# Kernel optimization log

Measured on AMD Instinct MI355X. Metric: run time of the kernel, lower is better.

Reference implementation:

```python
import jax, jax.numpy as jnp
import numpy as np

B, T, D, H, L = 2048, 512, 8, 20, 10  # batch, seq, input_dim, hidden_dim, num_layers


def setup_inputs() -> dict:
    key = jax.random.key(0)
    ks = jax.random.split(key, 10)
    s = 1.0 / np.sqrt(H)  # PyTorch nn.RNN / nn.Linear init bound
    u = lambda k, shape: jax.random.uniform(k, shape, jnp.float32, -s, s)
    return {
        "x": jax.random.normal(ks[0], (B, T, D), jnp.float32),
        "w_ih0": u(ks[1], (H, D)),        # layer-0 input weights
        "w_ih": u(ks[2], (L - 1, H, H)),  # layers 1..9 input weights
        "w_hh": u(ks[3], (L, H, H)),
        "b_ih": u(ks[4], (L, H)),
        "b_hh": u(ks[5], (L, H)),
        "fc_w": u(ks[6], (H, H)),
        "fc_b": u(ks[7], (H,)),
        "l2_w": u(ks[8], (1, H)),
        "l2_b": u(ks[9], (1,)),
    }


def reference(x, w_ih0, w_ih, w_hh, b_ih, b_hh, fc_w, fc_b, l2_w, l2_b):
    # 10-layer Elman RNN (tanh), batch_first, h0 = 0, eval mode (no dropout).
    Bn = x.shape[0]
    h0 = jnp.zeros((L, Bn, H), x.dtype)

    def step(h, x_t):  # h: [L, B, H], x_t: [B, D]
        hs = []
        inp = x_t
        for l in range(L):  # fixed small layer count -> unrolled
            Wi = w_ih0 if l == 0 else w_ih[l - 1]
            hl = jnp.tanh(inp @ Wi.T + b_ih[l] + h[l] @ w_hh[l].T + b_hh[l])
            hs.append(hl)
            inp = hl
        return jnp.stack(hs), hl  # carry, top-layer output

    _, out = jax.lax.scan(step, h0, jnp.swapaxes(x, 0, 1))  # out: [T, B, H]
    out = jnp.swapaxes(out, 0, 1)  # [B, T, H]
    # Time-independent MLP head (original loops over t; batched here, same math)
    y = jax.nn.relu(out @ fc_w.T + fc_b) @ l2_w.T + l2_b  # [B, T, 1]
    return y
```

## Files before the change

kernel.cpp:

```cpp
#include <hip/hip_runtime.h>

#if __has_builtin(__builtin_amdgcn_exp2f)
#define EXP2F(x) __builtin_amdgcn_exp2f(x)
#else
#define EXP2F(x) exp2f(x)
#endif
#if __has_builtin(__builtin_amdgcn_rcpf)
#define RCPF(x) __builtin_amdgcn_rcpf(x)
#else
#define RCPF(x) (1.0f / (x))
#endif

namespace {

constexpr int B_ = 2048, T_ = 512, D_ = 8, H_ = 20, L_ = 10;
constexpr int NG    = 16;
constexpr int PADK  = 40;
constexpr int NW    = 11;
constexpr int NTHR  = NW * 64;
constexpr int DEPTH = 8;
constexpr int SLOT_STRIDE  = L_ * NG * PADK;
constexpr int LAYER_STRIDE = NG * PADK;

typedef float f32x4 __attribute__((ext_vector_type(4)));
typedef short s16x8 __attribute__((ext_vector_type(8)));
typedef unsigned u32x4 __attribute__((ext_vector_type(4)));

#define LD4(p) (*reinterpret_cast<const f32x4*>(p))

__device__ __forceinline__ unsigned short f2bf(float f) {
    unsigned u = __builtin_bit_cast(unsigned, f);
    return (unsigned short)((u + 0x7FFFu + ((u >> 16) & 1u)) >> 16);
}
__device__ __forceinline__ float bf2f(unsigned short b) {
    return __builtin_bit_cast(float, (unsigned)b << 16);
}
__device__ __forceinline__ unsigned cvt_pk_bf16(float s0, float s1) {
    unsigned r;
    asm("v_cvt_pk_bf16_f32 %0, %1, %2" : "=v"(r) : "v"(s0), "v"(s1));
    return r;
}
__device__ __forceinline__ f32x4 mfma_bf16(s16x8 a, s16x8 b, f32x4 c) {
    return __builtin_amdgcn_mfma_f32_16x16x32_bf16(a, b, c, 0, 0, 0);
}
__device__ __forceinline__ float tanh_fast(float x) {
    float e = EXP2F(x * 2.8853900817779268f);
    return fmaf(-2.0f, RCPF(1.0f + e), 1.0f);
}

__device__ __forceinline__ int wait_ge_ret(int* p, int v) {
    int cur = __hip_atomic_load(p, __ATOMIC_ACQUIRE, __HIP_MEMORY_SCOPE_WORKGROUP);
    while (cur < v)
        cur = __hip_atomic_load(p, __ATOMIC_ACQUIRE, __HIP_MEMORY_SCOPE_WORKGROUP);
    __builtin_amdgcn_sched_barrier(0);
    return cur;
}
__device__ __forceinline__ void publish(int* p, int v) {
    asm volatile("s_waitcnt lgkmcnt(0)" ::: "memory");
    __hip_atomic_store(p, v, __ATOMIC_RELAXED, __HIP_MEMORY_SCOPE_WORKGROUP);
}

__device__ __forceinline__ s16x8 pack_x(f32x4 a, f32x4 b, bool lo) {
    s16x8 r;
    #pragma unroll
    for (int e = 0; e < 8; ++e) {
        float f = (e < 4) ? a[e] : b[e - 4];
        unsigned short hb = f2bf(f);
        r[e] = (short)(lo ? f2bf(f - bf2f(hb)) : hb);
    }
    return r;
}

__global__ __launch_bounds__(NTHR) void rnn_async(
    const float* __restrict__ x,
    const float* __restrict__ w_ih0,
    const float* __restrict__ w_ih,
    const float* __restrict__ w_hh,
    const float* __restrict__ b_ih,
    const float* __restrict__ b_hh,
    const float* __restrict__ fc_w,
    const float* __restrict__ fc_b,
    const float* __restrict__ l2_w,
    const float* __restrict__ l2_b,
    float* __restrict__ out)
{
    __shared__ __align__(16) unsigned short h_lds[DEPTH][L_][NG][PADK];
    __shared__ int prog[16];

    const int tid = threadIdx.x;
    const int w   = tid >> 6;
    const int l   = tid & 63;
    const int col = l & 15;
    const int g   = l >> 4;
    const int bg  = blockIdx.x * NG;

    {
        uint4* p4 = reinterpret_cast<uint4*>(&h_lds[0][0][0][0]);
        const int n4 = DEPTH * L_ * NG * PADK / 8;
        for (int i = tid; i < n4; i += NTHR) p4[i] = make_uint4(0, 0, 0, 0);
        if (tid < 16) prog[tid] = 0;
    }

    s16x8 a0_hi = {0,0,0,0,0,0,0,0}, a0_lo = a0_hi, a1_hi = a0_hi, a1_lo = a0_hi;
    s16x8 h0_hi = a0_hi, h0_lo = a0_hi, h1_hi = a0_hi, h1_lo = a0_hi;
    f32x4 bias0 = {0.f, 0.f, 0.f, 0.f}, bias1 = bias0;
    f32x4 l2v0 = bias0, l2v1 = bias0;
    float l2bv = 0.f;
    const bool mt1ok = col < (H_ - 16);

    if (w < L_) {
        const int layer = w;
        #pragma unroll
        for (int e = 0; e < 8; ++e) {
            const int k = g * 8 + e;
            float wv0 = 0.f, wv1 = 0.f;
            if (layer == 0) {
                if (k < 16) {
                    wv0 = w_ih0[col * D_ + (k & 7)];
                    if (mt1ok) wv1 = w_ih0[(16 + col) * D_ + (k & 7)];
                }
            } else if (k < H_) {
                wv0 = w_ih[((layer - 1) * H_ + col) * H_ + k];
                if (mt1ok) wv1 = w_ih[((layer - 1) * H_ + 16 + col) * H_ + k];
            }
            unsigned short b0 = f2bf(wv0), b1 = f2bf(wv1);
            a0_hi[e] = (short)b0; a0_lo[e] = (short)f2bf(wv0 - bf2f(b0));
            a1_hi[e] = (short)b1; a1_lo[e] = (short)f2bf(wv1 - bf2f(b1));
            float uv0 = 0.f, uv1 = 0.f;
            if (k < H_) {
                uv0 = w_hh[(layer * H_ + col) * H_ + k];
                if (mt1ok) uv1 = w_hh[(layer * H_ + 16 + col) * H_ + k];
            }
            unsigned short c0 = f2bf(uv0), c1 = f2bf(uv1);
            h0_hi[e] = (short)c0; h0_lo[e] = (short)f2bf(uv0 - bf2f(c0));
            h1_hi[e] = (short)c1; h1_lo[e] = (short)f2bf(uv1 - bf2f(c1));
        }
        #pragma unroll
        for (int r = 0; r < 4; ++r) {
            const int row = g * 4 + r;
            bias0[r] = b_ih[layer * H_ + row] + b_hh[layer * H_ + row];
            bias1[r] = (g == 0) ? (b_ih[layer * H_ + 16 + r] +
                                   b_hh[layer * H_ + 16 + r]) : 0.f;
        }
    } else {
        #pragma unroll
        for (int e = 0; e < 8; ++e) {
            const int k = g * 8 + e;
            float f0 = 0.f, f1 = 0.f;
            if (k < H_) {
                f0 = fc_w[col * H_ + k];
                if (mt1ok) f1 = fc_w[(16 + col) * H_ + k];
            }
            unsigned short b0 = f2bf(f0), b1 = f2bf(f1);
            a0_hi[e] = (short)b0; a0_lo[e] = (short)f2bf(f0 - bf2f(b0));
            a1_hi[e] = (short)b1; a1_lo[e] = (short)f2bf(f1 - bf2f(b1));
        }
        #pragma unroll
        for (int r = 0; r < 4; ++r) {
            bias0[r] = fc_b[g * 4 + r];
            bias1[r] = (g == 0) ? fc_b[16 + r] : 0.f;
            l2v0[r]  = l2_w[g * 4 + r];
            l2v1[r]  = (g == 0) ? l2_w[16 + r] : 0.f;
        }
        l2bv = l2_b[0];
    }

    const int i0 = (g == 1) ? col + 32 : col;
    const int i1 = (g == 0) ? col + 16 : ((g == 1) ? col + 48 : col);

    s16x8 xf_cur = {0,0,0,0,0,0,0,0}, xf_nxt = xf_cur;
    if (w == 0 && g < 2) {
        const float* xp = x + (size_t)(bg + col) * T_ * D_;
        xf_cur = pack_x(LD4(xp), LD4(xp + 4), g == 1);
        xf_nxt = pack_x(LD4(xp + D_), LD4(xp + D_ + 4), g == 1);
    }

    __syncthreads();

    unsigned short* const hb = &h_lds[0][0][0][0];
    const f32x4 z4 = {0.f, 0.f, 0.f, 0.f};

    if (w < L_) {
        const int rdB0 = (w ? (w - 1) * LAYER_STRIDE : 0) + col * PADK + g * 8;
        const int wr0  = w * LAYER_STRIDE + col * PADK + g * 4;
        const int wr1  = w * LAYER_STRIDE + col * PADK + 16;
        uint2 pw = make_uint2(0u, 0u), qw = pw;
        int p_up = 0, p_dn = 0;
        for (int t = 0; t < T_; ++t) {
            unsigned s0 = __shfl(pw.x, i0), s1 = __shfl(pw.y, i0);
            unsigned s2 = __shfl(pw.x, i1), s3 = __shfl(pw.y, i1);
            unsigned u0 = __shfl(qw.x, col), u1 = __shfl(qw.y, col);
            u32x4 bw;
            bw[0] = (g < 2) ? s0 : ((g == 2) ? u0 : 0u);
            bw[1] = (g < 2) ? s1 : ((g == 2) ? u1 : 0u);
            bw[2] = (g < 2) ? s2 : 0u;
            bw[3] = (g < 2) ? s3 : 0u;
            s16x8 B1 = __builtin_bit_cast(s16x8, bw);
            if (t > 0) {
                const int sp = ((t - 1) & (DEPTH - 1)) * SLOT_STRIDE;
                if (t - 1 >= DEPTH && p_dn < t - DEPTH)
                    p_dn = wait_ge_ret(&prog[w + 1], t - DEPTH);
                *reinterpret_cast<uint2*>(hb + sp + wr0) = pw;
                if (g == 0) *reinterpret_cast<uint2*>(hb + sp + wr1) = qw;
                if (l == 0) publish(&prog[w], t);
            }
            s16x8 B0;
            if (w == 0) {
                B0 = xf_cur;
                xf_cur = xf_nxt;
                if (g < 2 && t + 2 < T_) {
                    const float* xp = x + ((size_t)(bg + col) * T_ + t + 2) * D_;
                    xf_nxt = pack_x(LD4(xp), LD4(xp + 4), g == 1);
                }
            } else {
                if (p_up < t + 1) p_up = wait_ge_ret(&prog[w - 1], t + 1);
                B0 = *reinterpret_cast<const s16x8*>(
                    hb + (t & (DEPTH - 1)) * SLOT_STRIDE + rdB0);
            }
            f32x4 A  = mfma_bf16(h0_hi, B1, bias0);
            f32x4 Ab = mfma_bf16(h0_lo, B1, z4);
            f32x4 C  = mfma_bf16(h1_hi, B1, bias1);
            f32x4 Cb = mfma_bf16(h1_lo, B1, z4);
            A  = mfma_bf16(a0_hi, B0, A);
            Ab = mfma_bf16(a0_lo, B0, Ab);
            C  = mfma_bf16(a1_hi, B0, C);
            Cb = mfma_bf16(a1_lo, B0, Cb);
            f32x4 acc0 = A + Ab, acc1 = C + Cb;
            pw.x = cvt_pk_bf16(tanh_fast(acc0[0]), tanh_fast(acc0[1]));
            pw.y = cvt_pk_bf16(tanh_fast(acc0[2]), tanh_fast(acc0[3]));
            qw.x = cvt_pk_bf16(tanh_fast(acc1[0]), tanh_fast(acc1[1]));
            qw.y = cvt_pk_bf16(tanh_fast(acc1[2]), tanh_fast(acc1[3]));
        }
        {
            const int sp = ((T_ - 1) & (DEPTH - 1)) * SLOT_STRIDE;
            if (p_dn < T_ - DEPTH) wait_ge_ret(&prog[w + 1], T_ - DEPTH);
            *reinterpret_cast<uint2*>(hb + sp + wr0) = pw;
            if (g == 0) *reinterpret_cast<uint2*>(hb + sp + wr1) = qw;
            if (l == 0) publish(&prog[w], T_);
        }
    } else {
        const int rdH = (L_ - 1) * LAYER_STRIDE + col * PADK + g * 8;
        int p_up = 0;
        for (int t = 0; t < T_; ++t) {
            if (p_up < t + 1) p_up = wait_ge_ret(&prog[L_ - 1], t + 1);
            s16x8 Bh = *reinterpret_cast<const s16x8*>(
                hb + (t & (DEPTH - 1)) * SLOT_STRIDE + rdH);
            f32x4 z0  = mfma_bf16(a0_hi, Bh, bias0);
            f32x4 z0b = mfma_bf16(a0_lo, Bh, z4);
            f32x4 z1  = mfma_bf16(a1_hi, Bh, bias1);
            f32x4 z1b = mfma_bf16(a1_lo, Bh, z4);
            z0 += z0b; z1 += z1b;
            float part = 0.f;
            #pragma unroll
            for (int r = 0; r < 4; ++r) {
                part = fmaf(l2v0[r], fmaxf(z0[r], 0.f), part);
                part = fmaf(l2v1[r], fmaxf(z1[r], 0.f), part);
            }
            part += __shfl_xor(part, 16);
            part += __shfl_xor(part, 32);
            if (l < NG) out[(size_t)(bg + l) * T_ + t] = part + l2bv;
            if (l == 0) publish(&prog[L_], t + 1);
        }
    }
}

}

extern "C" void kernel_launch(void* const* d_in, const int* in_sizes, int n_in,
                              void* d_out, int out_size, void* d_ws, size_t ws_size,
                              hipStream_t stream) {
    const float* x     = (const float*)d_in[0];
    const float* w_ih0 = (const float*)d_in[1];
    const float* w_ih  = (const float*)d_in[2];
    const float* w_hh  = (const float*)d_in[3];
    const float* b_ih  = (const float*)d_in[4];
    const float* b_hh  = (const float*)d_in[5];
    const float* fc_w  = (const float*)d_in[6];
    const float* fc_b  = (const float*)d_in[7];
    const float* l2_w  = (const float*)d_in[8];
    const float* l2_b  = (const float*)d_in[9];
    float* out = (float*)d_out;

    const int grid = B_ / NG;
    hipLaunchKernelGGL(rnn_async, dim3(grid), dim3(NTHR), 0, stream,
                       x, w_ih0, w_ih, w_hh, b_ih, b_hh, fc_w, fc_b,
                       l2_w, l2_b, out);
}
```

Before: 368.7 us.

## Switch to 16x16x16 bf16 MFMA with register-resident recurrent operand and narrower LDS rows

Replaces the 16x16x32 MFMA, whose K=32 needed cross-lane shuffles to assemble the recurrent operand, with 16x16x16 MFMAs split into two K-tiles (0-15, 16-19). The previous step's tanh output is then fed directly as the B operand with no shuffles. LDS rows shrink from 40 to 24 elements, LDS writes move to the end of each step, and the spin-wait gains an s_sleep. The cost is more MFMA instructions per step (up to 16 instead of 8) and a possibly different LDS bank-conflict pattern.

```diff
diff --git a/kernel.cpp b/kernel.cpp
--- a/kernel.cpp
+++ b/kernel.cpp
@@ -15,7 +15,7 @@
 
 constexpr int B_ = 2048, T_ = 512, D_ = 8, H_ = 20, L_ = 10;
 constexpr int NG    = 16;
-constexpr int PADK  = 40;
+constexpr int PADK  = 24;
 constexpr int NW    = 11;
 constexpr int NTHR  = NW * 64;
 constexpr int DEPTH = 8;
@@ -23,8 +23,7 @@
 constexpr int LAYER_STRIDE = NG * PADK;
 
 typedef float f32x4 __attribute__((ext_vector_type(4)));
-typedef short s16x8 __attribute__((ext_vector_type(8)));
-typedef unsigned u32x4 __attribute__((ext_vector_type(4)));
+typedef short s16x4 __attribute__((ext_vector_type(4)));
 
 #define LD4(p) (*reinterpret_cast<const f32x4*>(p))
 
@@ -40,18 +39,34 @@
     asm("v_cvt_pk_bf16_f32 %0, %1, %2" : "=v"(r) : "v"(s0), "v"(s1));
     return r;
 }
-__device__ __forceinline__ f32x4 mfma_bf16(s16x8 a, s16x8 b, f32x4 c) {
-    return __builtin_amdgcn_mfma_f32_16x16x32_bf16(a, b, c, 0, 0, 0);
-}
 __device__ __forceinline__ float tanh_fast(float x) {
     float e = EXP2F(x * 2.8853900817779268f);
     return fmaf(-2.0f, RCPF(1.0f + e), 1.0f);
 }
 
+__device__ __forceinline__ f32x4 mfma16(s16x4 a, s16x4 b, f32x4 c) {
+    asm("v_mfma_f32_16x16x16_bf16 %0, %1, %2, %0"
+        : "+v"(c) : "v"(a), "v"(b));
+    return c;
+}
+
+struct AF { s16x4 hi, lo; };
+__device__ __forceinline__ AF mkfrag(float v0, float v1, float v2, float v3) {
+    AF f; float v[4] = {v0, v1, v2, v3};
+    #pragma unroll
+    for (int e = 0; e < 4; ++e) {
+        unsigned short h = f2bf(v[e]);
+        f.hi[e] = (short)h; f.lo[e] = (short)f2bf(v[e] - bf2f(h));
+    }
+    return f;
+}
+
 __device__ __forceinline__ int wait_ge_ret(int* p, int v) {
     int cur = __hip_atomic_load(p, __ATOMIC_ACQUIRE, __HIP_MEMORY_SCOPE_WORKGROUP);
-    while (cur < v)
+    while (cur < v) {
+        __builtin_amdgcn_s_sleep(1);
         cur = __hip_atomic_load(p, __ATOMIC_ACQUIRE, __HIP_MEMORY_SCOPE_WORKGROUP);
+    }
     __builtin_amdgcn_sched_barrier(0);
     return cur;
 }
@@ -60,28 +75,24 @@
     __hip_atomic_store(p, v, __ATOMIC_RELAXED, __HIP_MEMORY_SCOPE_WORKGROUP);
 }
 
-__device__ __forceinline__ s16x8 pack_x(f32x4 a, f32x4 b, bool lo) {
-    s16x8 r;
+__device__ __forceinline__ s16x4 pack_x4(f32x4 a, f32x4 b, int g) {
+    s16x4 r;
     #pragma unroll
-    for (int e = 0; e < 8; ++e) {
-        float f = (e < 4) ? a[e] : b[e - 4];
-        unsigned short hb = f2bf(f);
-        r[e] = (short)(lo ? f2bf(f - bf2f(hb)) : hb);
+    for (int e = 0; e < 4; ++e) {
+        int k = ((g & 1) << 2) + e;
+        float f = (k < 4) ? a[k] : b[k - 4];
+        unsigned short h = f2bf(f);
+        r[e] = (short)((g < 2) ? h : f2bf(f - bf2f(h)));
     }
     return r;
 }
 
 __global__ __launch_bounds__(NTHR) void rnn_async(
-    const float* __restrict__ x,
-    const float* __restrict__ w_ih0,
-    const float* __restrict__ w_ih,
-    const float* __restrict__ w_hh,
-    const float* __restrict__ b_ih,
-    const float* __restrict__ b_hh,
-    const float* __restrict__ fc_w,
-    const float* __restrict__ fc_b,
-    const float* __restrict__ l2_w,
-    const float* __restrict__ l2_b,
+    const float* __restrict__ x,      const float* __restrict__ w_ih0,
+    const float* __restrict__ w_ih,   const float* __restrict__ w_hh,
+    const float* __restrict__ b_ih,   const float* __restrict__ b_hh,
+    const float* __restrict__ fc_w,   const float* __restrict__ fc_b,
+    const float* __restrict__ l2_w,   const float* __restrict__ l2_b,
     float* __restrict__ out)
 {
     __shared__ __align__(16) unsigned short h_lds[DEPTH][L_][NG][PADK];
@@ -96,65 +107,65 @@
 
     {
         uint4* p4 = reinterpret_cast<uint4*>(&h_lds[0][0][0][0]);
-        const int n4 = DEPTH * L_ * NG * PADK / 8;
-        for (int i = tid; i < n4; i += NTHR) p4[i] = make_uint4(0, 0, 0, 0);
+        for (int i = tid; i < DEPTH * SLOT_STRIDE / 8; i += NTHR)
+            p4[i] = make_uint4(0, 0, 0, 0);
         if (tid < 16) prog[tid] = 0;
     }
 
-    s16x8 a0_hi = {0,0,0,0,0,0,0,0}, a0_lo = a0_hi, a1_hi = a0_hi, a1_lo = a0_hi;
-    s16x8 h0_hi = a0_hi, h0_lo = a0_hi, h1_hi = a0_hi, h1_lo = a0_hi;
-    f32x4 bias0 = {0.f, 0.f, 0.f, 0.f}, bias1 = bias0;
-    f32x4 l2v0 = bias0, l2v1 = bias0;
+    AF iA0, iA1, iB0, iB1;
+    AF hA0, hA1, hB0, hB1;
+    f32x4 bias0 = {0.f,0.f,0.f,0.f}, bias1 = bias0, l2v0 = bias0, l2v1 = bias0;
     float l2bv = 0.f;
-    const bool mt1ok = col < (H_ - 16);
+    const bool m1ok = col < 4;
+    const int k0 = g * 4;
 
     if (w < L_) {
-        const int layer = w;
-        #pragma unroll
-        for (int e = 0; e < 8; ++e) {
-            const int k = g * 8 + e;
-            float wv0 = 0.f, wv1 = 0.f;
-            if (layer == 0) {
-                if (k < 16) {
-                    wv0 = w_ih0[col * D_ + (k & 7)];
-                    if (mt1ok) wv1 = w_ih0[(16 + col) * D_ + (k & 7)];
-                }
-            } else if (k < H_) {
-                wv0 = w_ih[((layer - 1) * H_ + col) * H_ + k];
-                if (mt1ok) wv1 = w_ih[((layer - 1) * H_ + 16 + col) * H_ + k];
-            }
-            unsigned short b0 = f2bf(wv0), b1 = f2bf(wv1);
-            a0_hi[e] = (short)b0; a0_lo[e] = (short)f2bf(wv0 - bf2f(b0));
-            a1_hi[e] = (short)b1; a1_lo[e] = (short)f2bf(wv1 - bf2f(b1));
-            float uv0 = 0.f, uv1 = 0.f;
-            if (k < H_) {
-                uv0 = w_hh[(layer * H_ + col) * H_ + k];
-                if (mt1ok) uv1 = w_hh[(layer * H_ + 16 + col) * H_ + k];
-            }
-            unsigned short c0 = f2bf(uv0), c1 = f2bf(uv1);
-            h0_hi[e] = (short)c0; h0_lo[e] = (short)f2bf(uv0 - bf2f(c0));
-            h1_hi[e] = (short)c1; h1_lo[e] = (short)f2bf(uv1 - bf2f(c1));
-        }
+        if (w == 0) {
+            const int kx = ((g & 1) << 2);
+            const float* r0 = w_ih0 + col * D_ + kx;
+            iA0 = mkfrag(r0[0], r0[1], r0[2], r0[3]);
+            const float* r1 = w_ih0 + (16 + col) * D_ + kx;
+            iA1 = m1ok ? mkfrag(r1[0], r1[1], r1[2], r1[3]) : mkfrag(0,0,0,0);
+            iB0 = mkfrag(0,0,0,0); iB1 = mkfrag(0,0,0,0);
+        } else {
+            const float* Wm0 = w_ih + ((w - 1) * H_ + col) * H_;
+            const float* Wm1 = w_ih + ((w - 1) * H_ + 16 + col) * H_;
+            iA0 = mkfrag(Wm0[k0], Wm0[k0+1], Wm0[k0+2], Wm0[k0+3]);
+            iA1 = m1ok ? mkfrag(Wm1[k0], Wm1[k0+1], Wm1[k0+2], Wm1[k0+3])
+                       : mkfrag(0,0,0,0);
+            iB0 = (g == 0) ? mkfrag(Wm0[16], Wm0[17], Wm0[18], Wm0[19])
+                           : mkfrag(0,0,0,0);
+            iB1 = (g == 0 && m1ok)
+                           ? mkfrag(Wm1[16], Wm1[17], Wm1[18], Wm1[19])
+                           : mkfrag(0,0,0,0);
+        }
+        const float* Um0 = w_hh + (w * H_ + col) * H_;
+        const float* Um1 = w_hh + (w * H_ + 16 + col) * H_;
+        hA0 = mkfrag(Um0[k0], Um0[k0+1], Um0[k0+2], Um0[k0+3]);
+        hA1 = m1ok ? mkfrag(Um1[k0], Um1[k0+1], Um1[k0+2], Um1[k0+3])
+                   : mkfrag(0,0,0,0);
+        hB0 = (g == 0) ? mkfrag(Um0[16], Um0[17], Um0[18], Um0[19])
+                       : mkfrag(0,0,0,0);
+        hB1 = (g == 0 && m1ok) ? mkfrag(Um1[16], Um1[17], Um1[18], Um1[19])
+                               : mkfrag(0,0,0,0);
         #pragma unroll
         for (int r = 0; r < 4; ++r) {
             const int row = g * 4 + r;
-            bias0[r] = b_ih[layer * H_ + row] + b_hh[layer * H_ + row];
-            bias1[r] = (g == 0) ? (b_ih[layer * H_ + 16 + r] +
-                                   b_hh[layer * H_ + 16 + r]) : 0.f;
+            bias0[r] = b_ih[w * H_ + row] + b_hh[w * H_ + row];
+            bias1[r] = (g == 0) ? (b_ih[w * H_ + 16 + r] +
+                                   b_hh[w * H_ + 16 + r]) : 0.f;
         }
     } else {
-        #pragma unroll
-        for (int e = 0; e < 8; ++e) {
-            const int k = g * 8 + e;
-            float f0 = 0.f, f1 = 0.f;
-            if (k < H_) {
-                f0 = fc_w[col * H_ + k];
-                if (mt1ok) f1 = fc_w[(16 + col) * H_ + k];
-            }
-            unsigned short b0 = f2bf(f0), b1 = f2bf(f1);
-            a0_hi[e] = (short)b0; a0_lo[e] = (short)f2bf(f0 - bf2f(b0));
-            a1_hi[e] = (short)b1; a1_lo[e] = (short)f2bf(f1 - bf2f(b1));
-        }
+        const float* Fm0 = fc_w + col * H_;
+        const float* Fm1 = fc_w + (16 + col) * H_;
+        iA0 = mkfrag(Fm0[k0], Fm0[k0+1], Fm0[k0+2], Fm0[k0+3]);
+        iA1 = m1ok ? mkfrag(Fm1[k0], Fm1[k0+1], Fm1[k0+2], Fm1[k0+3])
+                   : mkfrag(0,0,0,0);
+        iB0 = (g == 0) ? mkfrag(Fm0[16], Fm0[17], Fm0[18], Fm0[19])
+                       : mkfrag(0,0,0,0);
+        iB1 = (g == 0 && m1ok) ? mkfrag(Fm1[16], Fm1[17], Fm1[18], Fm1[19])
+                               : mkfrag(0,0,0,0);
+        hA0 = hA1 = hB0 = hB1 = mkfrag(0,0,0,0);
         #pragma unroll
         for (int r = 0; r < 4; ++r) {
             bias0[r] = fc_b[g * 4 + r];
@@ -165,90 +176,93 @@
         l2bv = l2_b[0];
     }
 
-    const int i0 = (g == 1) ? col + 32 : col;
-    const int i1 = (g == 0) ? col + 16 : ((g == 1) ? col + 48 : col);
-
-    s16x8 xf_cur = {0,0,0,0,0,0,0,0}, xf_nxt = xf_cur;
-    if (w == 0 && g < 2) {
+    s16x4 xf_cur = {0,0,0,0}, xf_nxt = xf_cur;
+    if (w == 0) {
         const float* xp = x + (size_t)(bg + col) * T_ * D_;
-        xf_cur = pack_x(LD4(xp), LD4(xp + 4), g == 1);
-        xf_nxt = pack_x(LD4(xp + D_), LD4(xp + D_ + 4), g == 1);
+        xf_cur = pack_x4(LD4(xp), LD4(xp + 4), g);
+        xf_nxt = pack_x4(LD4(xp + D_), LD4(xp + D_ + 4), g);
     }
 
     __syncthreads();
 
     unsigned short* const hb = &h_lds[0][0][0][0];
     const f32x4 z4 = {0.f, 0.f, 0.f, 0.f};
+    const s16x4 zb = {0, 0, 0, 0};
 
     if (w < L_) {
-        const int rdB0 = (w ? (w - 1) * LAYER_STRIDE : 0) + col * PADK + g * 8;
+        const int rdB0 = (w ? (w - 1) * LAYER_STRIDE : 0) + col * PADK;
         const int wr0  = w * LAYER_STRIDE + col * PADK + g * 4;
         const int wr1  = w * LAYER_STRIDE + col * PADK + 16;
         uint2 pw = make_uint2(0u, 0u), qw = pw;
         int p_up = 0, p_dn = 0;
         for (int t = 0; t < T_; ++t) {
-            unsigned s0 = __shfl(pw.x, i0), s1 = __shfl(pw.y, i0);
-            unsigned s2 = __shfl(pw.x, i1), s3 = __shfl(pw.y, i1);
-            unsigned u0 = __shfl(qw.x, col), u1 = __shfl(qw.y, col);
-            u32x4 bw;
-            bw[0] = (g < 2) ? s0 : ((g == 2) ? u0 : 0u);
-            bw[1] = (g < 2) ? s1 : ((g == 2) ? u1 : 0u);
-            bw[2] = (g < 2) ? s2 : 0u;
-            bw[3] = (g < 2) ? s3 : 0u;
-            s16x8 B1 = __builtin_bit_cast(s16x8, bw);
-            if (t > 0) {
-                const int sp = ((t - 1) & (DEPTH - 1)) * SLOT_STRIDE;
-                if (t - 1 >= DEPTH && p_dn < t - DEPTH)
-                    p_dn = wait_ge_ret(&prog[w + 1], t - DEPTH);
-                *reinterpret_cast<uint2*>(hb + sp + wr0) = pw;
-                if (g == 0) *reinterpret_cast<uint2*>(hb + sp + wr1) = qw;
-                if (l == 0) publish(&prog[w], t);
-            }
-            s16x8 B0;
+            const int sc = (t & (DEPTH - 1)) * SLOT_STRIDE;
+            const s16x4 b1t0 = __builtin_bit_cast(s16x4, pw);
+            const s16x4 b1t1 = __builtin_bit_cast(s16x4, qw);
+            s16x4 b0t0, b0t1;
             if (w == 0) {
-                B0 = xf_cur;
+                b0t0 = xf_cur; b0t1 = zb;
                 xf_cur = xf_nxt;
-                if (g < 2 && t + 2 < T_) {
+                if (t + 2 < T_) {
                     const float* xp = x + ((size_t)(bg + col) * T_ + t + 2) * D_;
-                    xf_nxt = pack_x(LD4(xp), LD4(xp + 4), g == 1);
+                    xf_nxt = pack_x4(LD4(xp), LD4(xp + 4), g);
                 }
             } else {
                 if (p_up < t + 1) p_up = wait_ge_ret(&prog[w - 1], t + 1);
-                B0 = *reinterpret_cast<const s16x8*>(
-                    hb + (t & (DEPTH - 1)) * SLOT_STRIDE + rdB0);
+                const unsigned short* rp = hb + sc + rdB0;
+                b0t0 = __builtin_bit_cast(s16x4,
+                        *reinterpret_cast<const uint2*>(rp + g * 4));
+                b0t1 = (g == 0) ? __builtin_bit_cast(s16x4,
+                        *reinterpret_cast<const uint2*>(rp + 16)) : zb;
             }
-            f32x4 A  = mfma_bf16(h0_hi, B1, bias0);
-            f32x4 Ab = mfma_bf16(h0_lo, B1, z4);
-            f32x4 C  = mfma_bf16(h1_hi, B1, bias1);
-            f32x4 Cb = mfma_bf16(h1_lo, B1, z4);
-            A  = mfma_bf16(a0_hi, B0, A);
-            Ab = mfma_bf16(a0_lo, B0, Ab);
-            C  = mfma_bf16(a1_hi, B0, C);
-            Cb = mfma_bf16(a1_lo, B0, Cb);
-            f32x4 acc0 = A + Ab, acc1 = C + Cb;
-            pw.x = cvt_pk_bf16(tanh_fast(acc0[0]), tanh_fast(acc0[1]));
-            pw.y = cvt_pk_bf16(tanh_fast(acc0[2]), tanh_fast(acc0[3]));
+            f32x4 acc   = mfma16(iA0.hi, b0t0, bias0);
+            f32x4 acc1  = mfma16(iA1.hi, b0t0, bias1);
+            f32x4 accb  = mfma16(iA0.lo, b0t0, z4);
+            f32x4 acc1b = mfma16(iA1.lo, b0t0, z4);
+            if (w != 0) {
+                acc   = mfma16(iB0.hi, b0t1, acc);
+                acc1  = mfma16(iB1.hi, b0t1, acc1);
+                accb  = mfma16(iB0.lo, b0t1, accb);
+                acc1b = mfma16(iB1.lo, b0t1, acc1b);
+            }
+            acc   = mfma16(hA0.hi, b1t0, acc);
+            acc1  = mfma16(hA1.hi, b1t0, acc1);
+            accb  = mfma16(hA0.lo, b1t0, accb);
+            acc1b = mfma16(hA1.lo, b1t0, acc1b);
+            acc   = mfma16(hB0.hi, b1t1, acc);
+            acc1  = mfma16(hB1.hi, b1t1, acc1);
+            accb  = mfma16(hB0.lo, b1t1, accb);
+            acc1b = mfma16(hB1.lo, b1t1, acc1b);
+            acc += accb; acc1 += acc1b;
+            pw.x = cvt_pk_bf16(tanh_fast(acc[0]),  tanh_fast(acc[1]));
+            pw.y = cvt_pk_bf16(tanh_fast(acc[2]),  tanh_fast(acc[3]));
             qw.x = cvt_pk_bf16(tanh_fast(acc1[0]), tanh_fast(acc1[1]));
             qw.y = cvt_pk_bf16(tanh_fast(acc1[2]), tanh_fast(acc1[3]));
-        }
-        {
-            const int sp = ((T_ - 1) & (DEPTH - 1)) * SLOT_STRIDE;
-            if (p_dn < T_ - DEPTH) wait_ge_ret(&prog[w + 1], T_ - DEPTH);
-            *reinterpret_cast<uint2*>(hb + sp + wr0) = pw;
-            if (g == 0) *reinterpret_cast<uint2*>(hb + sp + wr1) = qw;
-            if (l == 0) publish(&prog[w], T_);
+            if (t >= DEPTH && p_dn < t - DEPTH + 1)
+                p_dn = wait_ge_ret(&prog[w + 1], t - DEPTH + 1);
+            *reinterpret_cast<uint2*>(hb + sc + wr0) = pw;
+            if (g == 0) *reinterpret_cast<uint2*>(hb + sc + wr1) = qw;
+            if (l == 0) publish(&prog[w], t + 1);
         }
     } else {
-        const int rdH = (L_ - 1) * LAYER_STRIDE + col * PADK + g * 8;
+        const int rdH = (L_ - 1) * LAYER_STRIDE + col * PADK;
         int p_up = 0;
         for (int t = 0; t < T_; ++t) {
             if (p_up < t + 1) p_up = wait_ge_ret(&prog[L_ - 1], t + 1);
-            s16x8 Bh = *reinterpret_cast<const s16x8*>(
-                hb + (t & (DEPTH - 1)) * SLOT_STRIDE + rdH);
-            f32x4 z0  = mfma_bf16(a0_hi, Bh, bias0);
-            f32x4 z0b = mfma_bf16(a0_lo, Bh, z4);
-            f32x4 z1  = mfma_bf16(a1_hi, Bh, bias1);
-            f32x4 z1b = mfma_bf16(a1_lo, Bh, z4);
+            const unsigned short* rp =
+                hb + (t & (DEPTH - 1)) * SLOT_STRIDE + rdH;
+            s16x4 bt0 = __builtin_bit_cast(s16x4,
+                    *reinterpret_cast<const uint2*>(rp + g * 4));
+            s16x4 bt1 = (g == 0) ? __builtin_bit_cast(s16x4,
+                    *reinterpret_cast<const uint2*>(rp + 16)) : zb;
+            f32x4 z0  = mfma16(iA0.hi, bt0, bias0);
+            f32x4 z1  = mfma16(iA1.hi, bt0, bias1);
+            f32x4 z0b = mfma16(iA0.lo, bt0, z4);
+            f32x4 z1b = mfma16(iA1.lo, bt0, z4);
+            z0  = mfma16(iB0.hi, bt1, z0);
+            z1  = mfma16(iB1.hi, bt1, z1);
+            z0b = mfma16(iB0.lo, bt1, z0b);
+            z1b = mfma16(iB1.lo, bt1, z1b);
             z0 += z0b; z1 += z1b;
             float part = 0.f;
             #pragma unroll
```

Result: slower. 414.1 us (+12.3%).
